# Kernel tuning notes

Measured on AMD Instinct MI355X. Metric: run time of the kernel, lower is better.

## Reference

```python
import jax, jax.numpy as jnp
import numpy as np

B, N, K, NB = 8, 4096, 16, 8
MAX_RADIUS = 10.0
OUT_MUL = 64  # irreps_out = '64x1o' -> output dim 64*3 = 192


def setup_inputs() -> dict:
    key = jax.random.key(0)
    k1, k2 = jax.random.split(key)
    coords = jax.random.normal(k1, (B, N, 3), dtype=jnp.float32)
    tp_weight = jax.random.normal(k2, (1, NB, OUT_MUL), dtype=jnp.float32)
    return {"coords": coords, "tp_weight": tp_weight}


def _knn_indices(coords, k):
    # coords: [B, N, 3] -> nbr idx [B, N, k] (no self loops), per-batch kNN
    n = coords.shape[1]
    d2 = jnp.sum((coords[:, :, None, :] - coords[:, None, :, :]) ** 2, axis=-1)  # [B,N,N]
    d2 = jnp.where(jnp.eye(n, dtype=bool)[None], jnp.inf, d2)
    _, idx = jax.lax.top_k(-d2, k)  # k nearest
    return idx


def reference(coords, tp_weight):
    nbr = _knn_indices(coords, K)                                # [B,N,K] int32
    nbr_coords = jax.vmap(lambda c, i: c[i])(coords, nbr)        # [B,N,K,3]
    r = nbr_coords - coords[:, :, None, :]                       # sender - receiver
    dist = jnp.linalg.norm(r, axis=-1, keepdims=True)            # [B,N,K,1]
    rhat = r / (dist + 1e-8)                                     # 1x1o input
    cutoff = jnp.clip(dist / MAX_RADIUS, 0.0, 1.0)
    # gaussian soft one-hot over [0,1] with NB centers
    centers = jnp.linspace(0.0, 1.0, NB, dtype=coords.dtype)
    sigma = 1.0 / NB
    g = jnp.exp(-((cutoff - centers) ** 2) / (2.0 * sigma * sigma))  # [B,N,K,NB]
    s = jnp.sum(g, axis=-1, keepdims=True)
    rb = g / jnp.where(s > 0, s, jnp.ones_like(s))               # 8x0e input
    # FullyConnectedTensorProduct 1x1o x NBx0e -> OUT_MULx1o (shared weights)
    # path normalization: 1/sqrt(mul_in1 * mul_in2) = 1/sqrt(NB)
    alpha = 1.0 / np.sqrt(1 * NB)
    W = tp_weight[0]                                             # [NB, OUT_MUL]
    edge_feat = alpha * jnp.einsum('vw,bnkv,bnkm->bnkwm', W, rb, rhat)  # [B,N,K,64,3]
    # exactly k incoming edges per receiver -> scatter_mean == mean over K
    agg = jnp.mean(edge_feat, axis=2).reshape(B, N, OUT_MUL * 3)  # [B,N,192]
    return agg
```

## Files before the change

### kernel.cpp

```cpp
#include <hip/hip_runtime.h>

typedef unsigned int u32;
typedef unsigned long long u64;
typedef float v2f __attribute__((ext_vector_type(2)));

#define NBATCH 8
#define NPTS   4096
#define NQTOT  (NBATCH * NPTS)
#define KNN    16
#define NBASIS 8
#define OUTM   64
#define NSPLIT 8
#define WIN    (NPTS / NSPLIT)
#define QPB    64
#define TKNN   (QPB * NSPLIT)
#define GRP    8
#define ECAP   64
#define ROWSTR 49
#define TOFF   32

#define SENT 0x7f800000ffffffffull

__device__ __forceinline__ void ce(u64& x, u64& y) {
  u64 a = x, b = y;
  bool sw = b < a;
  x = sw ? b : a;
  y = sw ? a : b;
}

template <int N>
__device__ __forceinline__ void oems_sort(u64* a) {
#pragma unroll
  for (int p = 1; p < N; p <<= 1) {
#pragma unroll
    for (int k = p; k >= 1; k >>= 1) {
#pragma unroll
      for (int j = k & (p - 1); j + k < N; j += 2 * k) {
#pragma unroll
        for (int i = 0; i < k; ++i) {
          int lo = i + j, hi = i + j + k;
          if (hi < N && (lo / (2 * p)) == (hi / (2 * p)))
            ce(a[lo], a[hi]);
        }
      }
    }
  }
}

__device__ __forceinline__ void merge16(u64 t[16], const u64 a[16]) {
  u64 m[16];
#pragma unroll
  for (int i = 0; i < 16; ++i) {
    u64 x = t[i], y = a[15 - i];
    m[i] = (x < y) ? x : y;
  }
#pragma unroll
  for (int k = 8; k >= 1; k >>= 1) {
#pragma unroll
    for (int i = 0; i < 16; ++i) {
      if ((i & k) == 0) ce(m[i], m[i | k]);
    }
  }
#pragma unroll
  for (int i = 0; i < 16; ++i) t[i] = m[i];
}

__device__ __forceinline__ v2f d2pair(v2f cx, v2f cy, v2f cz, v2f qx, v2f qy,
                                      v2f qz) {
#pragma clang fp contract(off)
  v2f dx = cx - qx;
  v2f dy = cy - qy;
  v2f dz = cz - qz;
  v2f d2 = (dx * dx + dy * dy) + dz * dz;
  return d2;
}

__device__ __forceinline__ float d2s(float cx, float cy, float cz, float qx,
                                     float qy, float qz) {
#pragma clang fp contract(off)
  float dx = cx - qx;
  float dy = cy - qy;
  float dz = cz - qz;
  return (dx * dx + dy * dy) + dz * dz;
}

__device__ __forceinline__ void pub16(u64* row, int seg, const u64 s[16]) {
#pragma unroll
  for (int e = 0; e < 16; ++e) row[seg * 16 + e] = s[e];
}

__device__ __forceinline__ void mrg16(const u64* row, int seg, u64 s[16]) {
  u64 a[16];
#pragma unroll
  for (int e = 0; e < 16; ++e) a[e] = row[seg * 16 + e];
  merge16(s, a);
}

__global__ __launch_bounds__(TKNN) void se3_kernel(
    const float* __restrict__ Xp, const float* __restrict__ Yp,
    const float* __restrict__ Zp, const float4* __restrict__ cpad,
    const float* __restrict__ Wmat, float* __restrict__ out) {
  __shared__ u64 sBuf[QPB * ROWSTR];
  __shared__ u32 sCnt[QPB];
  __shared__ float sThr[QPB];
  __shared__ float sM[QPB * 25];

  const int b = blockIdx.x;
  const int qg = blockIdx.y;
  const int tid = threadIdx.x;
  const int ql = tid & 63;
  const int sp = tid >> 6;
  const int qi = qg * QPB + ql;
  const int base = b * NPTS;

  if (tid < QPB) sCnt[tid] = 0;

  const float qx = Xp[base + qi];
  const float qy = Yp[base + qi];
  const float qz = Zp[base + qi];
  const v2f qxx = {qx, qx}, qyy = {qy, qy}, qzz = {qz, qz};

  const int wbase = __builtin_amdgcn_readfirstlane(sp * WIN);
  const v2f* xs2 = (const v2f*)(Xp + base + wbase);
  const v2f* ys2 = (const v2f*)(Yp + base + wbase);
  const v2f* zs2 = (const v2f*)(Zp + base + wbase);
  const int sj = qi - wbase;

  u64* row = sBuf + (size_t)ql * ROWSTR;

  {
    u64 s16[16];
    float cd[16];
#pragma unroll
    for (int p = 0; p < 8; ++p) {
      v2f d2 = d2pair(xs2[p], ys2[p], zs2[p], qxx, qyy, qzz);
      cd[2 * p + 0] = d2.x;
      cd[2 * p + 1] = d2.y;
    }
#pragma unroll
    for (int i = 0; i < 16; ++i) {
      u64 v = ((u64)__float_as_uint(cd[i]) << 32) | (u32)(wbase + i);
      s16[i] = (i == sj) ? SENT : v;
    }
    oems_sort<16>(s16);

    if (sp >= 5) pub16(row, sp - 5, s16);
    __syncthreads();
    if (sp >= 1 && sp <= 3) mrg16(row, sp - 1, s16);
    __syncthreads();
    if (sp == 4) pub16(row, 0, s16);
    if (sp == 3) pub16(row, 1, s16);
    __syncthreads();
    if (sp == 0) mrg16(row, 0, s16);
    if (sp == 1) mrg16(row, 1, s16);
    __syncthreads();
    if (sp == 2) pub16(row, 0, s16);
    if (sp == 1) pub16(row, 1, s16);
    __syncthreads();
    if (sp == 0) {
      mrg16(row, 0, s16);
      mrg16(row, 1, s16);
#pragma unroll
      for (int e = 0; e < 16; ++e) row[TOFF + e] = s16[e];
      sThr[ql] = __uint_as_float((u32)(s16[15] >> 32));
    }
    __syncthreads();
  }
  float thr = sThr[ql];

  const int selfgrp = (sj >= 0 && sj < WIN) ? (sj >> 3) : -1;
  const u32 selfbit = 1u << (sj & 7);

  u32* ebuf = (u32*)row;

#pragma unroll
  for (int ph = 0; ph < 5; ++ph) {
    const int cstart = 16 << ph;
    const int cend = 32 << ph;
#pragma unroll 2
    for (int g = cstart; g < cend; g += GRP) {
      v2f d2p[4];
#pragma unroll
      for (int p = 0; p < 4; ++p)
        d2p[p] = d2pair(xs2[(g >> 1) + p], ys2[(g >> 1) + p],
                        zs2[(g >> 1) + p], qxx, qyy, qzz);
      u32 want = 0;
#pragma unroll
      for (int i = 0; i < GRP; ++i)
        want |= (d2p[i >> 1][i & 1] <= thr) ? (1u << i) : 0u;
      if ((g >> 3) == selfgrp) want &= ~selfbit;
      if (want) {
        u32 slot = atomicAdd(&sCnt[ql], 1u);
        if (slot < ECAP) ebuf[slot] = (want << 12) | (u32)(wbase + g);
      }
    }
    __syncthreads();
    if (sp == ph + 1) {
      int n = (int)sCnt[ql];
      n = n < ECAP ? n : ECAP;
      if (__any(n > 0)) {
        u64 t16[16];
#pragma unroll
        for (int e = 0; e < 16; ++e) t16[e] = row[TOFF + e];
        int cursor = 0;
        u32 curWant = 0, curBase = 0;
        while (__any(cursor < n || curWant != 0)) {
          u32 kidx[16];
          u32 vmask = 0;
#pragma unroll
          for (int e = 0; e < 16; ++e) {
            if (curWant == 0 && cursor < n) {
              u32 ent = ebuf[cursor++];
              curWant = ent >> 12;
              curBase = ent & 0xFFFu;
            }
            if (curWant) {
              int bit = __ffs(curWant) - 1;
              curWant &= curWant - 1;
              kidx[e] = curBase + (u32)bit;
              vmask |= (1u << e);
            } else {
              kidx[e] = 0;
            }
          }
          u64 a[16];
#pragma unroll
          for (int e = 0; e < 16; ++e) {
            float4 c = cpad[base + (int)kidx[e]];
            float d2 = d2s(c.x, c.y, c.z, qx, qy, qz);
            u64 key = ((u64)__float_as_uint(d2) << 32) | kidx[e];
            a[e] = (vmask & (1u << e)) ? key : SENT;
          }
          oems_sort<16>(a);
          merge16(t16, a);
        }
#pragma unroll
        for (int e = 0; e < 16; ++e) row[TOFF + e] = t16[e];
        sThr[ql] = __uint_as_float((u32)(t16[15] >> 32));
      }
      sCnt[ql] = 0;
    }
    __syncthreads();
    thr = sThr[ql];
  }

  u64 pv[4];
  if (sp < 4) {
#pragma unroll
    for (int e = 0; e < 4; ++e) pv[e] = row[TOFF + sp * 4 + e];
  }
  __syncthreads();
  if (sp < 4) {
    const int k = sp;
    float4 nc[4];
    float dd[4];
#pragma unroll
    for (int e = 0; e < 4; ++e) {
      nc[e] = cpad[base + (int)(u32)pv[e]];
      dd[e] = __uint_as_float((u32)(pv[e] >> 32));
    }
    float M[24];
#pragma unroll
    for (int j = 0; j < 24; ++j) M[j] = 0.f;
#pragma unroll
    for (int e = 0; e < 4; ++e) {
      float rx = nc[e].x - qx;
      float ry = nc[e].y - qy;
      float rz = nc[e].z - qz;
      float dist = sqrtf(dd[e]);
      float inv = 1.0f / (dist + 1e-8f);
      rx *= inv; ry *= inv; rz *= inv;
      float cut = fminf(dist * 0.1f, 1.0f);
      float g[NBASIS], s = 0.f;
#pragma unroll
      for (int v = 0; v < NBASIS; ++v) {
        float t = cut - (float)v * (1.0f / 7.0f);
        g[v] = __expf(-32.0f * t * t);
        s += g[v];
      }
      float rs = 1.0f / s;
#pragma unroll
      for (int v = 0; v < NBASIS; ++v) {
        float rb = g[v] * rs;
        M[v * 3 + 0] = fmaf(rb, rx, M[v * 3 + 0]);
        M[v * 3 + 1] = fmaf(rb, ry, M[v * 3 + 1]);
        M[v * 3 + 2] = fmaf(rb, rz, M[v * 3 + 2]);
      }
    }
    float* fp = (float*)row;
#pragma unroll
    for (int c = 0; c < 24; ++c) fp[k * 24 + c] = M[c];
  }
  __syncthreads();

  {
    const float* fp = (const float*)row;
#pragma unroll
    for (int j0 = 0; j0 < 3; ++j0) {
      int j = sp * 3 + j0;
      float s = fp[0 * 24 + j] + fp[1 * 24 + j] + fp[2 * 24 + j] +
                fp[3 * 24 + j];
      sM[ql * 25 + j] = s;
    }
  }
  __syncthreads();

  float wreg[NBASIS];
#pragma unroll
  for (int v = 0; v < NBASIS; ++v) wreg[v] = Wmat[v * OUTM + ql];
  const float scale = 0.022097086912079608f;
#pragma unroll
  for (int i = 0; i < 8; ++i) {
    int q = sp * 8 + i;
    const float* mq = sM + q * 25;
    float a0 = 0.f, a1 = 0.f, a2 = 0.f;
#pragma unroll
    for (int v = 0; v < NBASIS; ++v) {
      a0 = fmaf(wreg[v], mq[v * 3 + 0], a0);
      a1 = fmaf(wreg[v], mq[v * 3 + 1], a1);
      a2 = fmaf(wreg[v], mq[v * 3 + 2], a2);
    }
    size_t o = (size_t)(base + qg * QPB + q) * (OUTM * 3) + ql * 3;
    out[o + 0] = a0 * scale;
    out[o + 1] = a1 * scale;
    out[o + 2] = a2 * scale;
  }
}

__global__ void prep_kernel(const float* __restrict__ coords,
                            float* __restrict__ Xp, float* __restrict__ Yp,
                            float* __restrict__ Zp, float4* __restrict__ cpad) {
  int i = blockIdx.x * 256 + threadIdx.x;
  if (i < NQTOT) {
    float x = coords[3 * i + 0];
    float y = coords[3 * i + 1];
    float z = coords[3 * i + 2];
    Xp[i] = x; Yp[i] = y; Zp[i] = z;
    cpad[i] = make_float4(x, y, z, 0.f);
  }
}

extern "C" void kernel_launch(void* const* d_in, const int* in_sizes, int n_in,
                              void* d_out, int out_size, void* d_ws, size_t ws_size,
                              hipStream_t stream) {
  const float* coords = (const float*)d_in[0];
  const float* Wmat = (const float*)d_in[1];
  float* out = (float*)d_out;

  char* w = (char*)d_ws;
  float* Xp = (float*)(w);
  float* Yp = (float*)(w + 131072);
  float* Zp = (float*)(w + 262144);
  float4* cpad = (float4*)(w + 393216);

  prep_kernel<<<dim3((NQTOT + 255) / 256), dim3(256), 0, stream>>>(coords, Xp, Yp, Zp, cpad);
  se3_kernel<<<dim3(NBATCH, NPTS / QPB), dim3(TKNN), 0, stream>>>(Xp, Yp, Zp, cpad, Wmat, out);
}
```

Before: 168.7 us.

## Split kNN search across two candidate halves with separate merge kernel

Splits the per-query candidate range into two halves processed by separate blocks (grid z dimension), each producing a partial top-16 that is written as 16-bit indices to a global buffer. A new merge kernel reloads both partial lists, recomputes distances, merges them, and runs the tensor-product aggregation. This doubles the number of blocks to improve GPU occupancy and shortens each block's serial scan. In exchange it adds a kernel launch, a global round-trip, and redundant distance recomputation.

```diff
diff --git a/kernel.cpp b/kernel.cpp
--- a/kernel.cpp
+++ b/kernel.cpp
@@ -1,5 +1,6 @@
 #include <hip/hip_runtime.h>
 
+typedef unsigned short u16;
 typedef unsigned int u32;
 typedef unsigned long long u64;
 typedef float v2f __attribute__((ext_vector_type(2)));
@@ -11,7 +12,8 @@
 #define NBASIS 8
 #define OUTM   64
 #define NSPLIT 8
-#define WIN    (NPTS / NSPLIT)
+#define NHALF  2
+#define WIN    (NPTS / (NSPLIT * NHALF))
 #define QPB    64
 #define TKNN   (QPB * NSPLIT)
 #define GRP    8
@@ -20,6 +22,8 @@
 #define TOFF   32
 
 #define SENT 0x7f800000ffffffffull
+
+__device__ u64 g_part[(size_t)NHALF * NQTOT * 4];
 
 __device__ __forceinline__ void ce(u64& x, u64& y) {
   u64 a = x, b = y;
@@ -98,15 +102,14 @@
 
 __global__ __launch_bounds__(TKNN) void se3_kernel(
     const float* __restrict__ Xp, const float* __restrict__ Yp,
-    const float* __restrict__ Zp, const float4* __restrict__ cpad,
-    const float* __restrict__ Wmat, float* __restrict__ out) {
+    const float* __restrict__ Zp, const float4* __restrict__ cpad) {
   __shared__ u64 sBuf[QPB * ROWSTR];
   __shared__ u32 sCnt[QPB];
   __shared__ float sThr[QPB];
-  __shared__ float sM[QPB * 25];
 
   const int b = blockIdx.x;
   const int qg = blockIdx.y;
+  const int z = blockIdx.z;
   const int tid = threadIdx.x;
   const int ql = tid & 63;
   const int sp = tid >> 6;
@@ -120,7 +123,7 @@
   const float qz = Zp[base + qi];
   const v2f qxx = {qx, qx}, qyy = {qy, qy}, qzz = {qz, qz};
 
-  const int wbase = __builtin_amdgcn_readfirstlane(sp * WIN);
+  const int wbase = __builtin_amdgcn_readfirstlane((z * NSPLIT + sp) * WIN);
   const v2f* xs2 = (const v2f*)(Xp + base + wbase);
   const v2f* ys2 = (const v2f*)(Yp + base + wbase);
   const v2f* zs2 = (const v2f*)(Zp + base + wbase);
@@ -174,7 +177,7 @@
   u32* ebuf = (u32*)row;
 
 #pragma unroll
-  for (int ph = 0; ph < 5; ++ph) {
+  for (int ph = 0; ph < 4; ++ph) {
     const int cstart = 16 << ph;
     const int cend = 32 << ph;
 #pragma unroll 2
@@ -244,6 +247,77 @@
     thr = sThr[ql];
   }
 
+  if (tid < 256) {
+    const int q = tid >> 2;
+    const int e0 = (tid & 3) * 4;
+    const u64* r = sBuf + (size_t)q * ROWSTR + TOFF;
+    u64 pk = 0;
+#pragma unroll
+    for (int e = 0; e < 4; ++e)
+      pk |= (u64)((u32)r[e0 + e] & 0xFFFFu) << (16 * e);
+    g_part[((size_t)z * NQTOT + base + qg * QPB + q) * 4 + (tid & 3)] = pk;
+  }
+}
+
+__global__ __launch_bounds__(TKNN) void knn_merge_kernel(
+    const float* __restrict__ Xp, const float* __restrict__ Yp,
+    const float* __restrict__ Zp, const float4* __restrict__ cpad,
+    const float* __restrict__ Wmat, float* __restrict__ out) {
+  __shared__ u64 sBuf[QPB * ROWSTR];
+  __shared__ u32 sIdx[QPB * 16];
+  __shared__ float sM[QPB * 25];
+
+  const int b = blockIdx.x;
+  const int qg = blockIdx.y;
+  const int tid = threadIdx.x;
+  const int ql = tid & 63;
+  const int sp = tid >> 6;
+  const int qi = qg * QPB + ql;
+  const int base = b * NPTS;
+
+  {
+    const u32* part32 = (const u32*)g_part;
+    const int q = tid >> 3;
+    const int s = tid & 7;
+#pragma unroll
+    for (int h = 0; h < NHALF; ++h) {
+      u32 v = part32[((size_t)h * NQTOT + base + qg * QPB + q) * 8 + s];
+      sIdx[q * 16 + h * 8 + s] = v;
+    }
+  }
+
+  const float qx = Xp[base + qi];
+  const float qy = Yp[base + qi];
+  const float qz = Zp[base + qi];
+
+  u64* row = sBuf + (size_t)ql * ROWSTR;
+  __syncthreads();
+
+  {
+    const u16* il = (const u16*)(sIdx + ql * 16);
+#pragma unroll
+    for (int e = 0; e < 4; ++e) {
+      int j = sp * 4 + e;
+      u32 idx = il[j];
+      float4 c = cpad[base + (int)idx];
+      float d2 = d2s(c.x, c.y, c.z, qx, qy, qz);
+      row[j] = ((u64)__float_as_uint(d2) << 32) | idx;
+    }
+  }
+  __syncthreads();
+
+  if (sp == 0) {
+    u64 t16[16], a[16];
+#pragma unroll
+    for (int e = 0; e < 16; ++e) t16[e] = row[e];
+#pragma unroll
+    for (int e = 0; e < 16; ++e) a[e] = row[16 + e];
+    merge16(t16, a);
+#pragma unroll
+    for (int e = 0; e < 16; ++e) row[TOFF + e] = t16[e];
+  }
+  __syncthreads();
+
   u64 pv[4];
   if (sp < 4) {
 #pragma unroll
@@ -353,6 +427,10 @@
   float* Zp = (float*)(w + 262144);
   float4* cpad = (float4*)(w + 393216);
 
-  prep_kernel<<<dim3((NQTOT + 255) / 256), dim3(256), 0, stream>>>(coords, Xp, Yp, Zp, cpad);
-  se3_kernel<<<dim3(NBATCH, NPTS / QPB), dim3(TKNN), 0, stream>>>(Xp, Yp, Zp, cpad, Wmat, out);
-}
+  prep_kernel<<<dim3((NQTOT + 255) / 256), dim3(256), 0, stream>>>(
+      coords, Xp, Yp, Zp, cpad);
+  se3_kernel<<<dim3(NBATCH, NPTS / QPB, NHALF), dim3(TKNN), 0, stream>>>(
+      Xp, Yp, Zp, cpad);
+  knn_merge_kernel<<<dim3(NBATCH, NPTS / QPB), dim3(TKNN), 0, stream>>>(
+      Xp, Yp, Zp, cpad, Wmat, out);
+}
```

Result: slower. 209.5 us (+24.2%).
